# Kernel tuning notes

Hardware: AMD Instinct MI355X
Metric: run time of the kernel (lower is better)

The kernel has to match this reference:

```python
import jax, jax.numpy as jnp
import numpy as np


def cosine_noise_schedule(t):
    # legacy mode: 1 - cos(t/1.008 * pi/2)^2
    return 1.0 - jnp.cos(t / 1.008 * jnp.pi / 2.0) ** 2


def setup_inputs() -> dict:
    key = jax.random.key(0)
    k1, k2, k3 = jax.random.split(key, 3)
    x = jax.random.normal(k1, (256, 3, 32, 32), dtype=jnp.float32)
    images = jax.random.normal(k2, (50000, 3, 32, 32), dtype=jnp.float32)
    t = jax.random.uniform(k3, (1,), dtype=jnp.float32)
    return {"t": t, "x": x, "images": images}


def reference(t, x, images):
    # Exact ideal score: softmax over dataset of Gaussian kernel weights.
    # The original streams dataset batches with an online-softmax running max;
    # with uniform batch sizes that is mathematically a global softmax over N:
    #   score = -(x - at * E_p[y]) / bt^2,  p_j = softmax(-||x - at*y_j||^2 / (2 bt^2))
    sched = cosine_noise_schedule(t)          # [1]
    bt = jnp.sqrt(sched)                      # [1]
    at = jnp.sqrt(1.0 - sched)                # [1]
    b, c, h, w = x.shape
    n = images.shape[0]
    xf = x.reshape(b, -1)                     # [b, chw]
    yf = images.reshape(n, -1)                # [n, chw]
    # ||x - at*y||^2 = ||x||^2 + at^2 ||y||^2 - 2 at x.y  (GEMM-dominant)
    x2 = jnp.sum(xf * xf, axis=1)             # [b]
    y2 = jnp.sum(yf * yf, axis=1)             # [n]
    cross = xf @ yf.T                         # [b, n]
    d2 = x2[:, None] + (at ** 2) * y2[None, :] - 2.0 * at * cross  # [b, n]
    logits = -d2 / (2.0 * bt ** 2)            # [b, n]
    p = jax.nn.softmax(logits, axis=1)        # [b, n], stable (max-subtracted)
    ybar = (p @ yf).reshape(b, c, h, w)       # softmax-weighted dataset mean
    return -(x - at * ybar) / (bt ** 2)
```

## Files before the change

### kernel.cpp

```cpp
#include <hip/hip_runtime.h>

typedef float    f32x4  __attribute__((ext_vector_type(4)));
typedef float    f32x16 __attribute__((ext_vector_type(16)));
typedef _Float16 f16x4  __attribute__((ext_vector_type(4)));
typedef _Float16 f16x8  __attribute__((ext_vector_type(8)));

#define N_IMG 50000
#define BROWS 256
#define CHW   3072
#define BK    64
#define BM    128
#define BN    128
#define EHS   50176
#define KCHUNK 3136
#define NSPLIT 16

__device__ __forceinline__ void glds16(const void* g, void* l) {
    __builtin_amdgcn_global_load_lds(
        (const __attribute__((address_space(1))) void*)g,
        (__attribute__((address_space(3))) void*)l, 16, 0, 0);
}

__global__ void k_scalars(const float* __restrict__ t, float* __restrict__ sc) {
    if (threadIdx.x == 0) {
        double tv  = (double)t[0];
        double ang = tv * (1.5707963267948966 / 1.008);
        double c   = cos(ang);
        double at  = c;
        double bt2 = 1.0 - c * c;
        sc[0] = (float)at;
        sc[1] = (float)bt2;
        sc[2] = (float)(at / bt2);
        sc[3] = (float)(at * at * 0.5 / bt2);
        sc[4] = (float)(1.0 / bt2);
    }
}

__global__ void k_xprep(const float* __restrict__ x, _Float16* __restrict__ xh) {
    int idx = blockIdx.x * 256 + threadIdx.x;
    f32x4 v = ((const f32x4*)x)[idx];
    f16x4 h;
    h[0] = (_Float16)v[0]; h[1] = (_Float16)v[1];
    h[2] = (_Float16)v[2]; h[3] = (_Float16)v[3];
    ((f16x4*)xh)[idx] = h;
}

__global__ void k_prep(const float* __restrict__ img, _Float16* __restrict__ imgh,
                       float* __restrict__ y2) {
    int row = blockIdx.x, tid = threadIdx.x;
    const f32x4* src = (const f32x4*)(img + (size_t)row * CHW);
    f16x4* dst = (f16x4*)(imgh + (size_t)row * CHW);
    float s = 0.f;
    #pragma unroll
    for (int i = 0; i < 3; i++) {
        f32x4 v = src[tid + i * 256];
        s += v[0]*v[0] + v[1]*v[1] + v[2]*v[2] + v[3]*v[3];
        f16x4 h;
        h[0] = (_Float16)v[0]; h[1] = (_Float16)v[1];
        h[2] = (_Float16)v[2]; h[3] = (_Float16)v[3];
        dst[tid + i * 256] = h;
    }
    for (int o = 32; o > 0; o >>= 1) s += __shfl_down(s, o);
    __shared__ float wsum[4];
    if ((tid & 63) == 0) wsum[tid >> 6] = s;
    __syncthreads();
    if (tid == 0) y2[row] = (wsum[0] + wsum[1]) + (wsum[2] + wsum[3]);
}

__global__ __launch_bounds__(256, 3) void k_gemm1(
        const _Float16* __restrict__ xh, const _Float16* __restrict__ imgh,
        const float* __restrict__ y2g, const float* __restrict__ sc,
        float* __restrict__ logits) {
    __shared__ _Float16 Alds[BM * BK];
    __shared__ _Float16 Blds[BN * BK];

    const int tid = threadIdx.x;
    const int wid = tid >> 6, lane = tid & 63;
    const int m0 = blockIdx.x * BM;
    const int n0 = blockIdx.y * BN;

    const _Float16* gA[4]; const _Float16* gB[4];
    _Float16* lA[4]; _Float16* lB[4];
    #pragma unroll
    for (int j = 0; j < 4; j++) {
        int seg = wid * 4 + j;
        int row = seg * 8 + (lane >> 3);
        int off = (((lane & 7) ^ (row & 7)) << 3);
        gA[j] = xh + (size_t)(m0 + row) * CHW + off;
        int rb = n0 + row; if (rb > N_IMG - 1) rb = N_IMG - 1;
        gB[j] = imgh + (size_t)rb * CHW + off;
        lA[j] = Alds + seg * 512;
        lB[j] = Blds + seg * 512;
    }

    const int wm = wid >> 1, wn = wid & 1;
    const int rm = wm * 64, cn = wn * 64;
    const int lr = lane & 31, hi = lane >> 5;
    const int xm = (lr & 7) << 4;
    const char* Ab = (const char*)Alds;
    const char* Bb = (const char*)Blds;
    const int ar0 = (rm + lr) * 128,      ar1 = (rm + 32 + lr) * 128;
    const int br0 = (cn + lr) * 128,      br1 = (cn + 32 + lr) * 128;
    const int kof = hi * 16;

    f32x16 acc[2][2];
    #pragma unroll
    for (int mi = 0; mi < 2; mi++)
        #pragma unroll
        for (int ni = 0; ni < 2; ni++)
            #pragma unroll
            for (int r = 0; r < 16; r++) acc[mi][ni][r] = 0.f;

    for (int it = 0; it < CHW / BK; ++it) {
        if (it) __syncthreads();
        #pragma unroll
        for (int j = 0; j < 4; j++) glds16(gA[j] + it * BK, lA[j]);
        #pragma unroll
        for (int j = 0; j < 4; j++) glds16(gB[j] + it * BK, lB[j]);
        __syncthreads();
        #pragma unroll
        for (int ks = 0; ks < 4; ++ks) {
            int off = (ks * 32 + kof) ^ xm;
            f16x8 a0 = *(const f16x8*)(Ab + ar0 + off);
            f16x8 a1 = *(const f16x8*)(Ab + ar1 + off);
            f16x8 b0 = *(const f16x8*)(Bb + br0 + off);
            f16x8 b1 = *(const f16x8*)(Bb + br1 + off);
            acc[0][0] = __builtin_amdgcn_mfma_f32_32x32x16_f16(a0, b0, acc[0][0], 0, 0, 0);
            acc[0][1] = __builtin_amdgcn_mfma_f32_32x32x16_f16(a0, b1, acc[0][1], 0, 0, 0);
            acc[1][0] = __builtin_amdgcn_mfma_f32_32x32x16_f16(a1, b0, acc[1][0], 0, 0, 0);
            acc[1][1] = __builtin_amdgcn_mfma_f32_32x32x16_f16(a1, b1, acc[1][1], 0, 0, 0);
        }
    }

    const float c_cross = sc[2], c_y2 = sc[3];
    #pragma unroll
    for (int mi = 0; mi < 2; mi++)
        #pragma unroll
        for (int ni = 0; ni < 2; ni++) {
            int col = n0 + cn + ni * 32 + lr;
            if (col >= N_IMG) continue;
            float y2v = y2g[col];
            f32x16 v = acc[mi][ni];
            #pragma unroll
            for (int r = 0; r < 16; r++) {
                int row = m0 + rm + mi * 32 + (r & 3) + 8 * (r >> 2) + 4 * hi;
                logits[(size_t)row * N_IMG + col] = c_cross * v[r] - c_y2 * y2v;
            }
        }
}

__global__ void k_softmax(const float* __restrict__ logits, _Float16* __restrict__ eh,
                          float* __restrict__ rowsum) {
    int row = blockIdx.x, tid = threadIdx.x;
    const f32x4* lr = (const f32x4*)(logits + (size_t)row * N_IMG);
    _Float16* erow = eh + (size_t)row * EHS;
    f16x4* er = (f16x4*)erow;
    __shared__ float wred[4];

    if (tid < EHS - N_IMG) erow[N_IMG + tid] = (_Float16)0.f;

    float m = -3.0e38f;
    for (int i = tid; i < N_IMG / 4; i += 256) {
        f32x4 v = lr[i];
        m = fmaxf(m, fmaxf(fmaxf(v[0], v[1]), fmaxf(v[2], v[3])));
    }
    for (int o = 32; o > 0; o >>= 1) m = fmaxf(m, __shfl_down(m, o));
    if ((tid & 63) == 0) wred[tid >> 6] = m;
    __syncthreads();
    m = fmaxf(fmaxf(wred[0], wred[1]), fmaxf(wred[2], wred[3]));
    __syncthreads();

    float s = 0.f;
    for (int i = tid; i < N_IMG / 4; i += 256) {
        f32x4 v = lr[i];
        float e0 = __expf(v[0] - m), e1 = __expf(v[1] - m);
        float e2 = __expf(v[2] - m), e3 = __expf(v[3] - m);
        s += (e0 + e1) + (e2 + e3);
        f16x4 h;
        h[0] = (_Float16)e0; h[1] = (_Float16)e1;
        h[2] = (_Float16)e2; h[3] = (_Float16)e3;
        er[i] = h;
    }
    for (int o = 32; o > 0; o >>= 1) s += __shfl_down(s, o);
    if ((tid & 63) == 0) wred[tid >> 6] = s;
    __syncthreads();
    if (tid == 0) rowsum[row] = (wred[0] + wred[1]) + (wred[2] + wred[3]);
}

__global__ __launch_bounds__(256, 3) void k_gemm2(
        const _Float16* __restrict__ eh, const _Float16* __restrict__ imgh,
        float* __restrict__ partial) {
    __shared__ _Float16 Alds[BM * BK];
    __shared__ _Float16 Blds[BN * 72];

    const int tid = threadIdx.x;
    const int wid = tid >> 6, lane = tid & 63;
    const int m0 = blockIdx.x * BM;
    const int d0 = blockIdx.y * BN;
    const int ck = blockIdx.z;
    const int kbase = ck * KCHUNK;
    const int kend  = (kbase + KCHUNK < N_IMG) ? (kbase + KCHUNK) : N_IMG;
    const int iters = (kend - kbase + BK - 1) / BK;

    const _Float16* gA[4]; _Float16* lA[4];
    #pragma unroll
    for (int j = 0; j < 4; j++) {
        int seg = wid * 4 + j;
        int row = seg * 8 + (lane >> 3);
        int off = (((lane & 7) ^ (row & 7)) << 3);
        gA[j] = eh + (size_t)(m0 + row) * EHS + kbase + off;
        lA[j] = Alds + seg * 512;
    }
    const int bd = (tid & 31) * 4;
    const int bq = (tid >> 5) * 8;
    f16x4 breg[8];
    auto loadB = [&](int kt) {
        #pragma unroll
        for (int i = 0; i < 8; i++) {
            int k = kt + bq + i; if (k > N_IMG - 1) k = N_IMG - 1;
            breg[i] = *(const f16x4*)(imgh + (size_t)k * CHW + d0 + bd);
        }
    };
    auto storeB = [&]() {
        #pragma unroll
        for (int j = 0; j < 4; j++) {
            f16x8 w;
            #pragma unroll
            for (int i = 0; i < 8; i++) w[i] = breg[i][j];
            *(f16x8*)&Blds[(bd + j) * 72 + bq] = w;
        }
    };

    const int wm = wid >> 1, wn = wid & 1;
    const int rm = wm * 64, cn = wn * 64;
    const int lr = lane & 31, hi = lane >> 5;
    const int xm = (lr & 7) << 4;
    const char* Ab = (const char*)Alds;
    const int ar0 = (rm + lr) * 128, ar1 = (rm + 32 + lr) * 128;
    const int kof = hi * 16;

    f32x16 acc[2][2];
    #pragma unroll
    for (int mi = 0; mi < 2; mi++)
        #pragma unroll
        for (int ni = 0; ni < 2; ni++)
            #pragma unroll
            for (int r = 0; r < 16; r++) acc[mi][ni][r] = 0.f;

    loadB(kbase);
    for (int it = 0; it < iters; ++it) {
        if (it) __syncthreads();
        #pragma unroll
        for (int j = 0; j < 4; j++) glds16(gA[j] + it * BK, lA[j]);
        storeB();
        __syncthreads();
        if (it + 1 < iters) loadB(kbase + (it + 1) * BK);
        #pragma unroll
        for (int ks = 0; ks < 4; ++ks) {
            int offa = (ks * 32 + kof) ^ xm;
            int offb = ks * 16 + hi * 8;
            f16x8 a0 = *(const f16x8*)(Ab + ar0 + offa);
            f16x8 a1 = *(const f16x8*)(Ab + ar1 + offa);
            f16x8 b0 = *(const f16x8*)&Blds[(cn +      lr) * 72 + offb];
            f16x8 b1 = *(const f16x8*)&Blds[(cn + 32 + lr) * 72 + offb];
            acc[0][0] = __builtin_amdgcn_mfma_f32_32x32x16_f16(a0, b0, acc[0][0], 0, 0, 0);
            acc[0][1] = __builtin_amdgcn_mfma_f32_32x32x16_f16(a0, b1, acc[0][1], 0, 0, 0);
            acc[1][0] = __builtin_amdgcn_mfma_f32_32x32x16_f16(a1, b0, acc[1][0], 0, 0, 0);
            acc[1][1] = __builtin_amdgcn_mfma_f32_32x32x16_f16(a1, b1, acc[1][1], 0, 0, 0);
        }
    }

    float* pp = partial + (size_t)ck * BROWS * CHW;
    #pragma unroll
    for (int mi = 0; mi < 2; mi++)
        #pragma unroll
        for (int ni = 0; ni < 2; ni++) {
            int dcol = d0 + cn + ni * 32 + lr;
            f32x16 v = acc[mi][ni];
            #pragma unroll
            for (int r = 0; r < 16; r++) {
                int row = m0 + rm + mi * 32 + (r & 3) + 8 * (r >> 2) + 4 * hi;
                pp[(size_t)row * CHW + dcol] = v[r];
            }
        }
}

__global__ void k_final(const float* __restrict__ partial, const float* __restrict__ x,
                        const float* __restrict__ rowsum, const float* __restrict__ sc,
                        float* __restrict__ out) {
    int idx = blockIdx.x * 256 + threadIdx.x;
    int row = idx / (CHW / 4);
    float at = sc[0], invbt2 = sc[4];
    float scale = at * invbt2 / rowsum[row];
    const f32x4* p4 = (const f32x4*)partial;
    f32x4 s = p4[idx];
    #pragma unroll
    for (int c = 1; c < NSPLIT; c++) s = s + p4[(size_t)c * (BROWS * CHW / 4) + idx];
    f32x4 xv = ((const f32x4*)x)[idx];
    f32x4 o;
    #pragma unroll
    for (int j = 0; j < 4; j++) o[j] = s[j] * scale - xv[j] * invbt2;
    ((f32x4*)out)[idx] = o;
}

extern "C" void kernel_launch(void* const* d_in, const int* in_sizes, int n_in,
                              void* d_out, int out_size, void* d_ws, size_t ws_size,
                              hipStream_t stream) {
    const float* t   = (const float*)d_in[0];
    const float* x   = (const float*)d_in[1];
    const float* img = (const float*)d_in[2];
    float* out = (float*)d_out;
    char* ws = (char*)d_ws;

    float*    sc     = (float*)(ws + 0);
    float*    rowsum = (float*)(ws + 256);
    float*    y2     = (float*)(ws + 4096);
    _Float16* xh     = (_Float16*)(ws + 212992);
    _Float16* imgh   = (_Float16*)(ws + 2097152);
    _Float16* eh     = (_Float16*)(ws + 311427072);
    float*    logits = (float*)(ws + 337117184);
    float*    partial = logits;

    k_scalars<<<1, 64, 0, stream>>>(t, sc);
    k_xprep<<<(BROWS * CHW / 4) / 256, 256, 0, stream>>>(x, xh);
    k_prep<<<N_IMG, 256, 0, stream>>>(img, imgh, y2);
    k_gemm1<<<dim3(2, (N_IMG + BN - 1) / BN), 256, 0, stream>>>(xh, imgh, y2, sc, logits);
    k_softmax<<<256, 256, 0, stream>>>(logits, eh, rowsum);
    k_gemm2<<<dim3(2, CHW / BN, NSPLIT), 256, 0, stream>>>(eh, imgh, partial);
    k_final<<<(BROWS * CHW / 4) / 256, 256, 0, stream>>>(partial, x, rowsum, sc, out);
}
```

Measured before the change: 490.3 us.

## Fuse fp16 image conversion and norm computation into both GEMM kernels

Removes the separate k_prep pass that converted the image dataset to fp16 and computed row norms. Instead, k_gemm1 and k_gemm2 read the fp32 images directly and convert to fp16 while staging into LDS, and k_gemm1 also accumulates the squared norms and reduces them per tile in shared memory. k_gemm1's B loads move from direct global-to-LDS copies to register prefetch of the next tile, overlapping with the MFMA loop. This drops one full write and read of the fp16 dataset and a launch, but each GEMM now reads twice as many bytes of B and uses more registers.

```diff
diff --git a/kernel.cpp b/kernel.cpp
--- a/kernel.cpp
+++ b/kernel.cpp
@@ -45,53 +45,60 @@
     ((f16x4*)xh)[idx] = h;
 }
 
-__global__ void k_prep(const float* __restrict__ img, _Float16* __restrict__ imgh,
-                       float* __restrict__ y2) {
-    int row = blockIdx.x, tid = threadIdx.x;
-    const f32x4* src = (const f32x4*)(img + (size_t)row * CHW);
-    f16x4* dst = (f16x4*)(imgh + (size_t)row * CHW);
-    float s = 0.f;
-    #pragma unroll
-    for (int i = 0; i < 3; i++) {
-        f32x4 v = src[tid + i * 256];
-        s += v[0]*v[0] + v[1]*v[1] + v[2]*v[2] + v[3]*v[3];
-        f16x4 h;
-        h[0] = (_Float16)v[0]; h[1] = (_Float16)v[1];
-        h[2] = (_Float16)v[2]; h[3] = (_Float16)v[3];
-        dst[tid + i * 256] = h;
-    }
-    for (int o = 32; o > 0; o >>= 1) s += __shfl_down(s, o);
-    __shared__ float wsum[4];
-    if ((tid & 63) == 0) wsum[tid >> 6] = s;
-    __syncthreads();
-    if (tid == 0) y2[row] = (wsum[0] + wsum[1]) + (wsum[2] + wsum[3]);
-}
-
 __global__ __launch_bounds__(256, 3) void k_gemm1(
-        const _Float16* __restrict__ xh, const _Float16* __restrict__ imgh,
-        const float* __restrict__ y2g, const float* __restrict__ sc,
-        float* __restrict__ logits) {
+        const _Float16* __restrict__ xh, const float* __restrict__ img,
+        const float* __restrict__ sc, float* __restrict__ logits) {
     __shared__ _Float16 Alds[BM * BK];
     __shared__ _Float16 Blds[BN * BK];
+    __shared__ float y2lds[BN];
 
     const int tid = threadIdx.x;
     const int wid = tid >> 6, lane = tid & 63;
     const int m0 = blockIdx.x * BM;
     const int n0 = blockIdx.y * BN;
 
-    const _Float16* gA[4]; const _Float16* gB[4];
-    _Float16* lA[4]; _Float16* lB[4];
+    const _Float16* gA[4]; _Float16* lA[4];
     #pragma unroll
     for (int j = 0; j < 4; j++) {
         int seg = wid * 4 + j;
         int row = seg * 8 + (lane >> 3);
         int off = (((lane & 7) ^ (row & 7)) << 3);
         gA[j] = xh + (size_t)(m0 + row) * CHW + off;
-        int rb = n0 + row; if (rb > N_IMG - 1) rb = N_IMG - 1;
-        gB[j] = imgh + (size_t)rb * CHW + off;
         lA[j] = Alds + seg * 512;
-        lB[j] = Blds + seg * 512;
-    }
+    }
+
+    const int brow = tid >> 3;
+    const int bg   = tid & 7;
+    const float* bsrc[4];
+    #pragma unroll
+    for (int i = 0; i < 4; i++) {
+        int r = n0 + brow + 32 * i; if (r > N_IMG - 1) r = N_IMG - 1;
+        bsrc[i] = img + (size_t)r * CHW + bg * 8;
+    }
+    const int bswz = ((bg ^ (brow & 7)) << 4);
+    f32x4 br[4][2];
+    float y2p[4] = {0.f, 0.f, 0.f, 0.f};
+
+    auto loadB = [&](int kt) {
+        #pragma unroll
+        for (int i = 0; i < 4; i++) {
+            br[i][0] = *(const f32x4*)(bsrc[i] + kt);
+            br[i][1] = *(const f32x4*)(bsrc[i] + kt + 4);
+        }
+    };
+    auto storeB = [&]() {
+        #pragma unroll
+        for (int i = 0; i < 4; i++) {
+            f16x8 h;
+            #pragma unroll
+            for (int j = 0; j < 4; j++) {
+                float a = br[i][0][j], b = br[i][1][j];
+                h[j] = (_Float16)a; h[4 + j] = (_Float16)b;
+                y2p[i] += a * a + b * b;
+            }
+            *(f16x8*)((char*)Blds + (brow + 32 * i) * 128 + bswz) = h;
+        }
+    };
 
     const int wm = wid >> 1, wn = wid & 1;
     const int rm = wm * 64, cn = wn * 64;
@@ -111,13 +118,14 @@
             #pragma unroll
             for (int r = 0; r < 16; r++) acc[mi][ni][r] = 0.f;
 
+    loadB(0);
     for (int it = 0; it < CHW / BK; ++it) {
         if (it) __syncthreads();
         #pragma unroll
         for (int j = 0; j < 4; j++) glds16(gA[j] + it * BK, lA[j]);
-        #pragma unroll
-        for (int j = 0; j < 4; j++) glds16(gB[j] + it * BK, lB[j]);
+        storeB();
         __syncthreads();
+        if (it + 1 < CHW / BK) loadB((it + 1) * BK);
         #pragma unroll
         for (int ks = 0; ks < 4; ++ks) {
             int off = (ks * 32 + kof) ^ xm;
@@ -132,6 +140,16 @@
         }
     }
 
+    #pragma unroll
+    for (int i = 0; i < 4; i++) {
+        float s = y2p[i];
+        s += __shfl_xor(s, 1);
+        s += __shfl_xor(s, 2);
+        s += __shfl_xor(s, 4);
+        if ((tid & 7) == 0) y2lds[brow + 32 * i] = s;
+    }
+    __syncthreads();
+
     const float c_cross = sc[2], c_y2 = sc[3];
     #pragma unroll
     for (int mi = 0; mi < 2; mi++)
@@ -139,7 +157,7 @@
         for (int ni = 0; ni < 2; ni++) {
             int col = n0 + cn + ni * 32 + lr;
             if (col >= N_IMG) continue;
-            float y2v = y2g[col];
+            float y2v = y2lds[cn + ni * 32 + lr];
             f32x16 v = acc[mi][ni];
             #pragma unroll
             for (int r = 0; r < 16; r++) {
@@ -188,7 +206,7 @@
 }
 
 __global__ __launch_bounds__(256, 3) void k_gemm2(
-        const _Float16* __restrict__ eh, const _Float16* __restrict__ imgh,
+        const _Float16* __restrict__ eh, const float* __restrict__ img,
         float* __restrict__ partial) {
     __shared__ _Float16 Alds[BM * BK];
     __shared__ _Float16 Blds[BN * 72];
@@ -213,12 +231,12 @@
     }
     const int bd = (tid & 31) * 4;
     const int bq = (tid >> 5) * 8;
-    f16x4 breg[8];
+    f32x4 breg[8];
     auto loadB = [&](int kt) {
         #pragma unroll
         for (int i = 0; i < 8; i++) {
             int k = kt + bq + i; if (k > N_IMG - 1) k = N_IMG - 1;
-            breg[i] = *(const f16x4*)(imgh + (size_t)k * CHW + d0 + bd);
+            breg[i] = *(const f32x4*)(img + (size_t)k * CHW + d0 + bd);
         }
     };
     auto storeB = [&]() {
@@ -226,7 +244,7 @@
         for (int j = 0; j < 4; j++) {
             f16x8 w;
             #pragma unroll
-            for (int i = 0; i < 8; i++) w[i] = breg[i][j];
+            for (int i = 0; i < 8; i++) w[i] = (_Float16)breg[i][j];
             *(f16x8*)&Blds[(bd + j) * 72 + bq] = w;
         }
     };
@@ -314,18 +332,15 @@
 
     float*    sc     = (float*)(ws + 0);
     float*    rowsum = (float*)(ws + 256);
-    float*    y2     = (float*)(ws + 4096);
-    _Float16* xh     = (_Float16*)(ws + 212992);
-    _Float16* imgh   = (_Float16*)(ws + 2097152);
-    _Float16* eh     = (_Float16*)(ws + 311427072);
-    float*    logits = (float*)(ws + 337117184);
+    _Float16* xh     = (_Float16*)(ws + 4096);
+    _Float16* eh     = (_Float16*)(ws + 2101248);
+    float*    logits = (float*)(ws + 27791360);
     float*    partial = logits;
 
     k_scalars<<<1, 64, 0, stream>>>(t, sc);
     k_xprep<<<(BROWS * CHW / 4) / 256, 256, 0, stream>>>(x, xh);
-    k_prep<<<N_IMG, 256, 0, stream>>>(img, imgh, y2);
-    k_gemm1<<<dim3(2, (N_IMG + BN - 1) / BN), 256, 0, stream>>>(xh, imgh, y2, sc, logits);
+    k_gemm1<<<dim3(2, (N_IMG + BN - 1) / BN), 256, 0, stream>>>(xh, img, sc, logits);
     k_softmax<<<256, 256, 0, stream>>>(logits, eh, rowsum);
-    k_gemm2<<<dim3(2, CHW / BN, NSPLIT), 256, 0, stream>>>(eh, imgh, partial);
+    k_gemm2<<<dim3(2, CHW / BN, NSPLIT), 256, 0, stream>>>(eh, img, partial);
     k_final<<<(BROWS * CHW / 4) / 256, 256, 0, stream>>>(partial, x, rowsum, sc, out);
 }
```

Result: no change. 484.7 us (-1.1%).

## Pre-transpose fp16 images in prep so gemm2 streams B via direct LDS loads

Applied to the files above, without the earlier changes.

The image prep kernel is retiled into 128x128 blocks. Besides the row-major fp16 copy, it now writes a transposed fp16 copy (CHW x padded N) through an LDS transpose, and accumulates the row norms with atomics after a memset. gemm2 then reads B from this transposed copy with swizzled global_load_lds, the same way it loads A. This removes the per-iteration register transpose and the strided B loads. In exchange it adds a second full-size fp16 write of the dataset, atomics on y2, and a larger workspace, and it drops the register prefetch of B that used to overlap with the MFMAs.

```diff
diff --git a/kernel.cpp b/kernel.cpp
--- a/kernel.cpp
+++ b/kernel.cpp
@@ -14,6 +14,7 @@
 #define EHS   50176
 #define KCHUNK 3136
 #define NSPLIT 16
+#define TPITCH 136
 
 __device__ __forceinline__ void glds16(const void* g, void* l) {
     __builtin_amdgcn_global_load_lds(
@@ -45,26 +46,42 @@
     ((f16x4*)xh)[idx] = h;
 }
 
-__global__ void k_prep(const float* __restrict__ img, _Float16* __restrict__ imgh,
-                       float* __restrict__ y2) {
-    int row = blockIdx.x, tid = threadIdx.x;
-    const f32x4* src = (const f32x4*)(img + (size_t)row * CHW);
-    f16x4* dst = (f16x4*)(imgh + (size_t)row * CHW);
-    float s = 0.f;
-    #pragma unroll
-    for (int i = 0; i < 3; i++) {
-        f32x4 v = src[tid + i * 256];
-        s += v[0]*v[0] + v[1]*v[1] + v[2]*v[2] + v[3]*v[3];
+__global__ __launch_bounds__(256) void k_prep(const float* __restrict__ img,
+        _Float16* __restrict__ imgh, _Float16* __restrict__ imgT,
+        float* __restrict__ y2) {
+    __shared__ _Float16 LT[128 * TPITCH];
+    const int tid = threadIdx.x;
+    const int n0 = blockIdx.x * 128;
+    const int d0 = blockIdx.y * 128;
+    const int rbase = tid >> 5;
+    const int dcol  = (tid & 31) * 4;
+
+    for (int i = 0; i < 16; i++) {
+        int nl = rbase + i * 8;
+        int n  = n0 + nl;
+        bool valid = n < N_IMG;
+        int nc = valid ? n : (N_IMG - 1);
+        f32x4 v = *(const f32x4*)(img + (size_t)nc * CHW + d0 + dcol);
+        if (!valid) { v[0] = 0.f; v[1] = 0.f; v[2] = 0.f; v[3] = 0.f; }
+        float s = v[0]*v[0] + v[1]*v[1] + v[2]*v[2] + v[3]*v[3];
+        s += __shfl_xor(s, 1); s += __shfl_xor(s, 2); s += __shfl_xor(s, 4);
+        s += __shfl_xor(s, 8); s += __shfl_xor(s, 16);
+        if ((tid & 31) == 0 && valid) atomicAdd(&y2[n], s);
         f16x4 h;
         h[0] = (_Float16)v[0]; h[1] = (_Float16)v[1];
         h[2] = (_Float16)v[2]; h[3] = (_Float16)v[3];
-        dst[tid + i * 256] = h;
-    }
-    for (int o = 32; o > 0; o >>= 1) s += __shfl_down(s, o);
-    __shared__ float wsum[4];
-    if ((tid & 63) == 0) wsum[tid >> 6] = s;
+        if (valid) *(f16x4*)(imgh + (size_t)n * CHW + d0 + dcol) = h;
+        #pragma unroll
+        for (int j = 0; j < 4; j++) LT[(dcol + j) * TPITCH + nl] = h[j];
+    }
     __syncthreads();
-    if (tid == 0) y2[row] = (wsum[0] + wsum[1]) + (wsum[2] + wsum[3]);
+
+    const int dl = tid >> 1;
+    const int nh = (tid & 1) * 64;
+    const f16x8* src = (const f16x8*)&LT[dl * TPITCH + nh];
+    f16x8* dst = (f16x8*)(imgT + (size_t)(d0 + dl) * EHS + n0 + nh);
+    #pragma unroll
+    for (int g = 0; g < 8; g++) dst[g] = src[g];
 }
 
 __global__ __launch_bounds__(256, 3) void k_gemm1(
@@ -188,55 +205,38 @@
 }
 
 __global__ __launch_bounds__(256, 3) void k_gemm2(
-        const _Float16* __restrict__ eh, const _Float16* __restrict__ imgh,
+        const _Float16* __restrict__ eh, const _Float16* __restrict__ imgT,
         float* __restrict__ partial) {
     __shared__ _Float16 Alds[BM * BK];
-    __shared__ _Float16 Blds[BN * 72];
+    __shared__ _Float16 Blds[BN * BK];
 
     const int tid = threadIdx.x;
     const int wid = tid >> 6, lane = tid & 63;
     const int m0 = blockIdx.x * BM;
     const int d0 = blockIdx.y * BN;
-    const int ck = blockIdx.z;
-    const int kbase = ck * KCHUNK;
-    const int kend  = (kbase + KCHUNK < N_IMG) ? (kbase + KCHUNK) : N_IMG;
-    const int iters = (kend - kbase + BK - 1) / BK;
-
-    const _Float16* gA[4]; _Float16* lA[4];
+    const int kbase = blockIdx.z * KCHUNK;
+
+    const _Float16* gA[4]; const _Float16* gB[4];
+    _Float16* lA[4]; _Float16* lB[4];
     #pragma unroll
     for (int j = 0; j < 4; j++) {
         int seg = wid * 4 + j;
         int row = seg * 8 + (lane >> 3);
         int off = (((lane & 7) ^ (row & 7)) << 3);
-        gA[j] = eh + (size_t)(m0 + row) * EHS + kbase + off;
+        gA[j] = eh   + (size_t)(m0 + row) * EHS + kbase + off;
+        gB[j] = imgT + (size_t)(d0 + row) * EHS + kbase + off;
         lA[j] = Alds + seg * 512;
-    }
-    const int bd = (tid & 31) * 4;
-    const int bq = (tid >> 5) * 8;
-    f16x4 breg[8];
-    auto loadB = [&](int kt) {
-        #pragma unroll
-        for (int i = 0; i < 8; i++) {
-            int k = kt + bq + i; if (k > N_IMG - 1) k = N_IMG - 1;
-            breg[i] = *(const f16x4*)(imgh + (size_t)k * CHW + d0 + bd);
-        }
-    };
-    auto storeB = [&]() {
-        #pragma unroll
-        for (int j = 0; j < 4; j++) {
-            f16x8 w;
-            #pragma unroll
-            for (int i = 0; i < 8; i++) w[i] = breg[i][j];
-            *(f16x8*)&Blds[(bd + j) * 72 + bq] = w;
-        }
-    };
+        lB[j] = Blds + seg * 512;
+    }
 
     const int wm = wid >> 1, wn = wid & 1;
     const int rm = wm * 64, cn = wn * 64;
     const int lr = lane & 31, hi = lane >> 5;
     const int xm = (lr & 7) << 4;
     const char* Ab = (const char*)Alds;
-    const int ar0 = (rm + lr) * 128, ar1 = (rm + 32 + lr) * 128;
+    const char* Bb = (const char*)Blds;
+    const int ar0 = (rm + lr) * 128,      ar1 = (rm + 32 + lr) * 128;
+    const int br0 = (cn + lr) * 128,      br1 = (cn + 32 + lr) * 128;
     const int kof = hi * 16;
 
     f32x16 acc[2][2];
@@ -247,22 +247,20 @@
             #pragma unroll
             for (int r = 0; r < 16; r++) acc[mi][ni][r] = 0.f;
 
-    loadB(kbase);
-    for (int it = 0; it < iters; ++it) {
+    for (int it = 0; it < KCHUNK / BK; ++it) {
         if (it) __syncthreads();
         #pragma unroll
         for (int j = 0; j < 4; j++) glds16(gA[j] + it * BK, lA[j]);
-        storeB();
+        #pragma unroll
+        for (int j = 0; j < 4; j++) glds16(gB[j] + it * BK, lB[j]);
         __syncthreads();
-        if (it + 1 < iters) loadB(kbase + (it + 1) * BK);
         #pragma unroll
         for (int ks = 0; ks < 4; ++ks) {
-            int offa = (ks * 32 + kof) ^ xm;
-            int offb = ks * 16 + hi * 8;
-            f16x8 a0 = *(const f16x8*)(Ab + ar0 + offa);
-            f16x8 a1 = *(const f16x8*)(Ab + ar1 + offa);
-            f16x8 b0 = *(const f16x8*)&Blds[(cn +      lr) * 72 + offb];
-            f16x8 b1 = *(const f16x8*)&Blds[(cn + 32 + lr) * 72 + offb];
+            int off = (ks * 32 + kof) ^ xm;
+            f16x8 a0 = *(const f16x8*)(Ab + ar0 + off);
+            f16x8 a1 = *(const f16x8*)(Ab + ar1 + off);
+            f16x8 b0 = *(const f16x8*)(Bb + br0 + off);
+            f16x8 b1 = *(const f16x8*)(Bb + br1 + off);
             acc[0][0] = __builtin_amdgcn_mfma_f32_32x32x16_f16(a0, b0, acc[0][0], 0, 0, 0);
             acc[0][1] = __builtin_amdgcn_mfma_f32_32x32x16_f16(a0, b1, acc[0][1], 0, 0, 0);
             acc[1][0] = __builtin_amdgcn_mfma_f32_32x32x16_f16(a1, b0, acc[1][0], 0, 0, 0);
@@ -270,7 +268,7 @@
         }
     }
 
-    float* pp = partial + (size_t)ck * BROWS * CHW;
+    float* pp = partial + (size_t)blockIdx.z * BROWS * CHW;
     #pragma unroll
     for (int mi = 0; mi < 2; mi++)
         #pragma unroll
@@ -317,15 +315,17 @@
     float*    y2     = (float*)(ws + 4096);
     _Float16* xh     = (_Float16*)(ws + 212992);
     _Float16* imgh   = (_Float16*)(ws + 2097152);
-    _Float16* eh     = (_Float16*)(ws + 311427072);
-    float*    logits = (float*)(ws + 337117184);
+    _Float16* imgT   = (_Float16*)(ws + 309297152);
+    _Float16* eh     = (_Float16*)(ws + 617578496);
+    float*    logits = (float*)(ws + 643268608);
     float*    partial = logits;
 
     k_scalars<<<1, 64, 0, stream>>>(t, sc);
     k_xprep<<<(BROWS * CHW / 4) / 256, 256, 0, stream>>>(x, xh);
-    k_prep<<<N_IMG, 256, 0, stream>>>(img, imgh, y2);
+    hipMemsetAsync(y2, 0, N_IMG * sizeof(float), stream);
+    k_prep<<<dim3((N_IMG + 127) / 128, CHW / 128), 256, 0, stream>>>(img, imgh, imgT, y2);
     k_gemm1<<<dim3(2, (N_IMG + BN - 1) / BN), 256, 0, stream>>>(xh, imgh, y2, sc, logits);
     k_softmax<<<256, 256, 0, stream>>>(logits, eh, rowsum);
-    k_gemm2<<<dim3(2, CHW / BN, NSPLIT), 256, 0, stream>>>(eh, imgh, partial);
+    k_gemm2<<<dim3(2, CHW / BN, NSPLIT), 256, 0, stream>>>(eh, imgT, partial);
     k_final<<<(BROWS * CHW / 4) / 256, 256, 0, stream>>>(partial, x, rowsum, sc, out);
 }
```

After: 630.2 us. 1.29x slower.

## Pad image matrix, remap blocks per XCD, async double-buffer B loads in gemm2

Applied to the files above, without the earlier changes.

The image matrix is zero-padded to a multiple of the tile so both GEMMs can drop bounds clamping. Both GEMMs map their flat grid so each XCD works on a contiguous slice of the image rows or K-chunks, which should improve L2 locality. In gemm2, the B operand is now fetched with global_load_lds into a staging buffer and transposed through LDS into a swizzled layout, and A is double-buffered so the next tile's loads overlap the MFMA loop. LDS use goes up and occupancy drops to 2 blocks per CU, and the in-LDS transpose adds extra shared-memory traffic and barriers.

```diff
diff --git a/kernel.cpp b/kernel.cpp
--- a/kernel.cpp
+++ b/kernel.cpp
@@ -6,6 +6,7 @@
 typedef _Float16 f16x8  __attribute__((ext_vector_type(8)));
 
 #define N_IMG 50000
+#define NPAD  50176
 #define BROWS 256
 #define CHW   3072
 #define BK    64
@@ -48,8 +49,14 @@
 __global__ void k_prep(const float* __restrict__ img, _Float16* __restrict__ imgh,
                        float* __restrict__ y2) {
     int row = blockIdx.x, tid = threadIdx.x;
+    f16x4* dst = (f16x4*)(imgh + (size_t)row * CHW);
+    if (row >= N_IMG) {
+        f16x4 z = {(_Float16)0.f, (_Float16)0.f, (_Float16)0.f, (_Float16)0.f};
+        #pragma unroll
+        for (int i = 0; i < 3; i++) dst[tid + i * 256] = z;
+        return;
+    }
     const f32x4* src = (const f32x4*)(img + (size_t)row * CHW);
-    f16x4* dst = (f16x4*)(imgh + (size_t)row * CHW);
     float s = 0.f;
     #pragma unroll
     for (int i = 0; i < 3; i++) {
@@ -76,8 +83,10 @@
 
     const int tid = threadIdx.x;
     const int wid = tid >> 6, lane = tid & 63;
-    const int m0 = blockIdx.x * BM;
-    const int n0 = blockIdx.y * BN;
+    const int flat = blockIdx.x;
+    const int xcd = flat & 7, loc = flat >> 3;
+    const int m0 = (loc & 1) * BM;
+    const int n0 = (xcd * 49 + (loc >> 1)) * BN;
 
     const _Float16* gA[4]; const _Float16* gB[4];
     _Float16* lA[4]; _Float16* lB[4];
@@ -187,56 +196,42 @@
     if (tid == 0) rowsum[row] = (wred[0] + wred[1]) + (wred[2] + wred[3]);
 }
 
-__global__ __launch_bounds__(256, 3) void k_gemm2(
+__global__ __launch_bounds__(256, 2) void k_gemm2(
         const _Float16* __restrict__ eh, const _Float16* __restrict__ imgh,
         float* __restrict__ partial) {
-    __shared__ _Float16 Alds[BM * BK];
-    __shared__ _Float16 Blds[BN * 72];
+    __shared__ _Float16 Alds[2][BM * BK];
+    __shared__ _Float16 Blds[BN * BK];
+    __shared__ _Float16 Tmp[BK * BN];
 
     const int tid = threadIdx.x;
     const int wid = tid >> 6, lane = tid & 63;
-    const int m0 = blockIdx.x * BM;
-    const int d0 = blockIdx.y * BN;
-    const int ck = blockIdx.z;
+    const int flat = blockIdx.x;
+    const int xcd = flat & 7, loc = flat >> 3;
+    const int ck  = xcd * 2 + (loc >= 48 ? 1 : 0);
+    const int rem = loc - (loc >= 48 ? 48 : 0);
+    const int m0 = (rem & 1) * BM;
+    const int d0 = (rem >> 1) * BN;
     const int kbase = ck * KCHUNK;
-    const int kend  = (kbase + KCHUNK < N_IMG) ? (kbase + KCHUNK) : N_IMG;
-    const int iters = (kend - kbase + BK - 1) / BK;
-
-    const _Float16* gA[4]; _Float16* lA[4];
+
+    const _Float16* gA[4]; int lAo[4];
+    const _Float16* gB[4]; _Float16* lB[4];
     #pragma unroll
     for (int j = 0; j < 4; j++) {
         int seg = wid * 4 + j;
         int row = seg * 8 + (lane >> 3);
         int off = (((lane & 7) ^ (row & 7)) << 3);
         gA[j] = eh + (size_t)(m0 + row) * EHS + kbase + off;
-        lA[j] = Alds + seg * 512;
-    }
-    const int bd = (tid & 31) * 4;
-    const int bq = (tid >> 5) * 8;
-    f16x4 breg[8];
-    auto loadB = [&](int kt) {
-        #pragma unroll
-        for (int i = 0; i < 8; i++) {
-            int k = kt + bq + i; if (k > N_IMG - 1) k = N_IMG - 1;
-            breg[i] = *(const f16x4*)(imgh + (size_t)k * CHW + d0 + bd);
-        }
-    };
-    auto storeB = [&]() {
-        #pragma unroll
-        for (int j = 0; j < 4; j++) {
-            f16x8 w;
-            #pragma unroll
-            for (int i = 0; i < 8; i++) w[i] = breg[i][j];
-            *(f16x8*)&Blds[(bd + j) * 72 + bq] = w;
-        }
-    };
+        lAo[j] = seg * 512;
+        gB[j] = imgh + (size_t)(kbase + seg * 4 + (lane >> 4)) * CHW + d0 + (lane & 15) * 8;
+        lB[j] = Tmp + seg * 512;
+    }
 
     const int wm = wid >> 1, wn = wid & 1;
     const int rm = wm * 64, cn = wn * 64;
     const int lr = lane & 31, hi = lane >> 5;
     const int xm = (lr & 7) << 4;
-    const char* Ab = (const char*)Alds;
     const int ar0 = (rm + lr) * 128, ar1 = (rm + 32 + lr) * 128;
+    const int br0 = (cn + lr) * 128, br1 = (cn + 32 + lr) * 128;
     const int kof = hi * 16;
 
     f32x16 acc[2][2];
@@ -247,27 +242,47 @@
             #pragma unroll
             for (int r = 0; r < 16; r++) acc[mi][ni][r] = 0.f;
 
-    loadB(kbase);
-    for (int it = 0; it < iters; ++it) {
-        if (it) __syncthreads();
-        #pragma unroll
-        for (int j = 0; j < 4; j++) glds16(gA[j] + it * BK, lA[j]);
-        storeB();
+    #pragma unroll
+    for (int j = 0; j < 4; j++) glds16(gA[j], (_Float16*)Alds[0] + lAo[j]);
+    #pragma unroll
+    for (int j = 0; j < 4; j++) glds16(gB[j], lB[j]);
+
+    int c = 0;
+    for (int it = 0; it < KCHUNK / BK; ++it) {
         __syncthreads();
-        if (it + 1 < iters) loadB(kbase + (it + 1) * BK);
+        #pragma unroll
+        for (int tt = 0; tt < 4; tt++) {
+            int gid = tid + tt * 256;
+            int d = gid & 127, oct = gid >> 7;
+            f16x8 w;
+            #pragma unroll
+            for (int j = 0; j < 8; j++) w[j] = Tmp[(oct * 8 + j) * 128 + d];
+            *(f16x8*)((char*)Blds + d * 128 + ((oct ^ (d & 7)) << 4)) = w;
+        }
+        __syncthreads();
+        if (it + 1 < KCHUNK / BK) {
+            #pragma unroll
+            for (int j = 0; j < 4; j++)
+                glds16(gA[j] + (it + 1) * BK, (_Float16*)Alds[c ^ 1] + lAo[j]);
+            #pragma unroll
+            for (int j = 0; j < 4; j++)
+                glds16(gB[j] + (size_t)(it + 1) * BK * CHW, lB[j]);
+        }
+        const char* Ab = (const char*)Alds[c];
+        const char* Bb = (const char*)Blds;
         #pragma unroll
         for (int ks = 0; ks < 4; ++ks) {
-            int offa = (ks * 32 + kof) ^ xm;
-            int offb = ks * 16 + hi * 8;
-            f16x8 a0 = *(const f16x8*)(Ab + ar0 + offa);
-            f16x8 a1 = *(const f16x8*)(Ab + ar1 + offa);
-            f16x8 b0 = *(const f16x8*)&Blds[(cn +      lr) * 72 + offb];
-            f16x8 b1 = *(const f16x8*)&Blds[(cn + 32 + lr) * 72 + offb];
+            int off = (ks * 32 + kof) ^ xm;
+            f16x8 a0 = *(const f16x8*)(Ab + ar0 + off);
+            f16x8 a1 = *(const f16x8*)(Ab + ar1 + off);
+            f16x8 b0 = *(const f16x8*)(Bb + br0 + off);
+            f16x8 b1 = *(const f16x8*)(Bb + br1 + off);
             acc[0][0] = __builtin_amdgcn_mfma_f32_32x32x16_f16(a0, b0, acc[0][0], 0, 0, 0);
             acc[0][1] = __builtin_amdgcn_mfma_f32_32x32x16_f16(a0, b1, acc[0][1], 0, 0, 0);
             acc[1][0] = __builtin_amdgcn_mfma_f32_32x32x16_f16(a1, b0, acc[1][0], 0, 0, 0);
             acc[1][1] = __builtin_amdgcn_mfma_f32_32x32x16_f16(a1, b1, acc[1][1], 0, 0, 0);
         }
+        c ^= 1;
     }
 
     float* pp = partial + (size_t)ck * BROWS * CHW;
@@ -317,15 +332,15 @@
     float*    y2     = (float*)(ws + 4096);
     _Float16* xh     = (_Float16*)(ws + 212992);
     _Float16* imgh   = (_Float16*)(ws + 2097152);
-    _Float16* eh     = (_Float16*)(ws + 311427072);
-    float*    logits = (float*)(ws + 337117184);
+    _Float16* eh     = (_Float16*)(ws + 310378496);
+    float*    logits = (float*)(ws + 336068608);
     float*    partial = logits;
 
     k_scalars<<<1, 64, 0, stream>>>(t, sc);
     k_xprep<<<(BROWS * CHW / 4) / 256, 256, 0, stream>>>(x, xh);
-    k_prep<<<N_IMG, 256, 0, stream>>>(img, imgh, y2);
-    k_gemm1<<<dim3(2, (N_IMG + BN - 1) / BN), 256, 0, stream>>>(xh, imgh, y2, sc, logits);
+    k_prep<<<NPAD, 256, 0, stream>>>(img, imgh, y2);
+    k_gemm1<<<784, 256, 0, stream>>>(xh, imgh, y2, sc, logits);
     k_softmax<<<256, 256, 0, stream>>>(logits, eh, rowsum);
-    k_gemm2<<<dim3(2, CHW / BN, NSPLIT), 256, 0, stream>>>(eh, imgh, partial);
+    k_gemm2<<<768, 256, 0, stream>>>(eh, imgh, partial);
     k_final<<<(BROWS * CHW / 4) / 256, 256, 0, stream>>>(partial, x, rowsum, sc, out);
 }
```

Result: slower. 524.5 us (+7.0%).
